# Kernel tuning notes

Measured on AMD Instinct MI355X. Metric: run time of the kernel, lower is better.

The kernel has to match this reference:

```python
import jax, jax.numpy as jnp
import numpy as np

N_NODES = 100000
N_EDGES = 3200000
N_GRAPHS = 128


def setup_inputs() -> dict:
    key = jax.random.key(0)
    ks = jax.random.split(key, 16)
    x = jax.random.normal(ks[0], (N_NODES, 47), dtype=jnp.float32)
    edge_index = jax.random.randint(ks[1], (2, N_EDGES), 0, N_NODES, dtype=jnp.int32)
    batch = jnp.sort(jax.random.randint(ks[2], (N_NODES,), 0, N_GRAPHS, dtype=jnp.int32))

    def w(k, shape):
        fan_in = shape[0]
        return jax.random.normal(k, shape, dtype=jnp.float32) * (1.0 / np.sqrt(fan_in))

    return {
        "x": x, "edge_index": edge_index, "batch": batch,
        "W1": w(ks[3], (47, 64)), "b1": jnp.zeros((64,), jnp.float32),
        "W2": w(ks[4], (64, 32)), "b2": jnp.zeros((32,), jnp.float32),
        "A1": w(ks[5], (32, 32)), "c1": jnp.zeros((32,), jnp.float32),
        "A2": w(ks[6], (32, 16)), "c2": jnp.zeros((16,), jnp.float32),
        "A3": w(ks[7], (16, 8)),  "c3": jnp.zeros((8,), jnp.float32),
        "A4": w(ks[8], (8, 1)),   "c4": jnp.zeros((1,), jnp.float32),
    }


def _gcn_conv(x, W, b, src, dst):
    # PyG GCNConv: h = XW, then D^-1/2 (A+I) D^-1/2 aggregation, then + bias.
    h = x @ W  # [N, out]
    ones = jnp.ones(dst.shape[0], dtype=h.dtype)
    deg = jax.ops.segment_sum(ones, dst, num_segments=N_NODES)  # incl. self loops
    dinv = jnp.where(deg > 0, jax.lax.rsqrt(deg), 0.0)
    norm = dinv[src] * dinv[dst]  # [E_total]
    msg = h[src] * norm[:, None]  # gather + normalize
    out = jax.ops.segment_sum(msg, dst, num_segments=N_NODES)  # scatter-add
    return out + b


def reference(x, edge_index, batch, W1, b1, W2, b2, A1, c1, A2, c2, A3, c3, A4, c4):
    loops = jnp.arange(N_NODES, dtype=edge_index.dtype)
    src = jnp.concatenate([edge_index[0], loops])
    dst = jnp.concatenate([edge_index[1], loops])
    h = jax.nn.relu(_gcn_conv(x, W1, b1, src, dst))
    h = jax.nn.relu(_gcn_conv(h, W2, b2, src, dst))
    # dropout is identity in eval mode
    g = jax.ops.segment_sum(h, batch, num_segments=N_GRAPHS)  # global_add_pool [G,32]
    g = jax.nn.relu(g @ A1 + c1)
    g = jax.nn.relu(g @ A2 + c2)
    g = jax.nn.relu(g @ A3 + c3)
    return g @ A4 + c4  # [G, 1]
```

## Files before the change

### kernel.cpp

```cpp
#include <hip/hip_runtime.h>

#define N_NODES 100000
#define N_EDGES 3200000
#define N_GRAPHS 128

#define RSHIFT 8
#define NPR 256
#define R_RANGES ((N_NODES + NPR - 1) / NPR)
#define CAP 9472
#define C_CHUNKS 512
#define EPC (N_EDGES / C_CHUNKS)
#define SRC_BITS 17

#define XPB 64
#define AXW 48

__device__ inline unsigned short f2bf(float f) {
    unsigned u = __float_as_uint(f);
    unsigned r = u + 0x7FFFu + ((u >> 16) & 1u);
    return (unsigned short)(r >> 16);
}
__device__ inline float bflo(unsigned u) { return __uint_as_float(u << 16); }
__device__ inline float bfhi(unsigned u) { return __uint_as_float(u & 0xFFFF0000u); }


__global__ __launch_bounds__(256) void padcvt_kernel(const float* __restrict__ x,
                                                     unsigned short* __restrict__ xpb,
                                                     int* __restrict__ range_next) {
    if (blockIdx.x < 2) {
        int i = blockIdx.x * 256 + threadIdx.x;
        if (i < R_RANGES) range_next[i] = i * CAP;
    }
    int idx = blockIdx.x * 256 + threadIdx.x;
    if (idx >= N_NODES * XPB) return;
    int n = idx >> 6;
    int c = idx & 63;
    float v = (c < 47) ? x[n * 47 + c] : 0.f;
    xpb[idx] = f2bf(v);
}


__global__ __launch_bounds__(256) void partition_kernel(const int* __restrict__ src,
                                                        const int* __restrict__ dst,
                                                        int* __restrict__ range_next,
                                                        int* __restrict__ bucket) {
    __shared__ int sorted[EPC];
    __shared__ unsigned short rid[EPC];
    __shared__ int cntL[R_RANGES];
    __shared__ int lstart[R_RANGES];
    __shared__ int baseL[R_RANGES];
    __shared__ int scanbuf[256];
    const int t = threadIdx.x, b = blockIdx.x;
    const int e0 = b * EPC;
    for (int i = t; i < R_RANGES; i += 256) cntL[i] = 0;
    __syncthreads();
    for (int i = t; i < EPC; i += 256) atomicAdd(&cntL[dst[e0 + i] >> RSHIFT], 1);
    __syncthreads();
    int i0 = 2 * t, i1 = 2 * t + 1;
    int v0 = (i0 < R_RANGES) ? cntL[i0] : 0;
    int v1 = (i1 < R_RANGES) ? cntL[i1] : 0;
    int s = v0 + v1;
    scanbuf[t] = s;
    __syncthreads();
    for (int d = 1; d < 256; d <<= 1) {
        int tv = (t >= d) ? scanbuf[t - d] : 0;
        __syncthreads();
        scanbuf[t] += tv;
        __syncthreads();
    }
    int ex = scanbuf[t] - s;
    if (i0 < R_RANGES) {
        lstart[i0] = ex;
        baseL[i0] = (v0 > 0) ? atomicAdd(&range_next[i0], v0) : 0;
        cntL[i0] = 0;
    }
    if (i1 < R_RANGES) {
        lstart[i1] = ex + v0;
        baseL[i1] = (v1 > 0) ? atomicAdd(&range_next[i1], v1) : 0;
        cntL[i1] = 0;
    }
    __syncthreads();
    for (int i = t; i < EPC; i += 256) {
        int d = dst[e0 + i];
        int sv = src[e0 + i];
        int r = d >> RSHIFT;
        int q = lstart[r] + atomicAdd(&cntL[r], 1);
        sorted[q] = ((d & (NPR - 1)) << SRC_BITS) | sv;
        rid[q] = (unsigned short)r;
    }
    __syncthreads();
    for (int i = t; i < EPC; i += 256) {
        int r = rid[i];
        bucket[baseL[r] + (i - lstart[r])] = sorted[i];
    }
}


__global__ __launch_bounds__(256) void build_kernel(const int* __restrict__ bucket,
                                                    const int* __restrict__ range_next,
                                                    int* __restrict__ row_ptr,
                                                    int* __restrict__ row_cnt,
                                                    float* __restrict__ dinv,
                                                    int* __restrict__ csr_src) {
    __shared__ int sE[CAP];
    __shared__ int degs[NPR];
    __shared__ int part[256];
    const int t = threadIdx.x, r = blockIdx.x;
    const int base_node = r * NPR;
    const int seg0 = r * CAP;
    int m = range_next[r] - seg0;
    if (m > CAP) m = CAP;
    for (int i = t; i < m; i += 256) sE[i] = bucket[seg0 + i];
    degs[t] = 0;
    __syncthreads();
    for (int i = t; i < m; i += 256) atomicAdd(&degs[sE[i] >> SRC_BITS], 1);
    __syncthreads();
    int d = degs[t];
    part[t] = d;
    __syncthreads();
    for (int dd = 1; dd < 256; dd <<= 1) {
        int tv = (t >= dd) ? part[t - dd] : 0;
        __syncthreads();
        part[t] += tv;
        __syncthreads();
    }
    int ex = part[t] - d;
    int node = base_node + t;
    if (node < N_NODES) {
        row_ptr[node] = seg0 + ex;
        row_cnt[node] = d;
        dinv[node] = rsqrtf((float)(d + 1));
    }
    degs[t] = ex;
    __syncthreads();
    for (int i = t; i < m; i += 256) {
        int p = sE[i];
        int pos = atomicAdd(&degs[p >> SRC_BITS], 1);
        csr_src[seg0 + pos] = p & ((1 << SRC_BITS) - 1);
    }
}


__global__ __launch_bounds__(256) void wprep_kernel(const int* __restrict__ csr_src,
                                                    const int* __restrict__ range_next,
                                                    const float* __restrict__ dinv,
                                                    float* __restrict__ csr_w) {
    const int t = threadIdx.x, r = blockIdx.x;
    const int seg0 = r * CAP;
    int m = range_next[r] - seg0;
    if (m > CAP) m = CAP;
    for (int i = t; i < m; i += 256) {
        csr_w[seg0 + i] = dinv[csr_src[seg0 + i]];
    }
}


__global__ __launch_bounds__(256) void aggX_kernel(const unsigned short* __restrict__ xpb,
                                                   const float* __restrict__ dinv,
                                                   const int* __restrict__ row_ptr,
                                                   const int* __restrict__ row_cnt,
                                                   const int* __restrict__ csr_src,
                                                   const float* __restrict__ csr_w,
                                                   unsigned short* __restrict__ aggxb) {
    const int tid = threadIdx.x;
    const int n = blockIdx.x * 4 + (tid >> 6);
    if (n >= N_NODES) return;
    const int l = tid & 63;
    const int eo = l >> 3;
    const int cg = l & 7;
    const float dn = dinv[n];

    float acc[8] = {0.f, 0.f, 0.f, 0.f, 0.f, 0.f, 0.f, 0.f};
    if (eo == 0) {
        uint4 q = *(const uint4*)(xpb + (size_t)n * XPB + cg * 8);
        float w = dn * dn;
        acc[0] = bflo(q.x) * w; acc[1] = bfhi(q.x) * w;
        acc[2] = bflo(q.y) * w; acc[3] = bfhi(q.y) * w;
        acc[4] = bflo(q.z) * w; acc[5] = bfhi(q.z) * w;
        acc[6] = bflo(q.w) * w; acc[7] = bfhi(q.w) * w;
    }
    const int st = row_ptr[n];
    const int cnt = row_cnt[n];
    int k = eo;
    for (; k + 8 < cnt; k += 16) {
        int s0 = csr_src[st + k];
        int s1 = csr_src[st + k + 8];
        float w0 = csr_w[st + k] * dn;
        float w1 = csr_w[st + k + 8] * dn;
        uint4 q0 = *(const uint4*)(xpb + (size_t)s0 * XPB + cg * 8);
        uint4 q1 = *(const uint4*)(xpb + (size_t)s1 * XPB + cg * 8);
        acc[0] = fmaf(bflo(q0.x), w0, acc[0]); acc[1] = fmaf(bfhi(q0.x), w0, acc[1]);
        acc[2] = fmaf(bflo(q0.y), w0, acc[2]); acc[3] = fmaf(bfhi(q0.y), w0, acc[3]);
        acc[4] = fmaf(bflo(q0.z), w0, acc[4]); acc[5] = fmaf(bfhi(q0.z), w0, acc[5]);
        acc[6] = fmaf(bflo(q0.w), w0, acc[6]); acc[7] = fmaf(bfhi(q0.w), w0, acc[7]);
        acc[0] = fmaf(bflo(q1.x), w1, acc[0]); acc[1] = fmaf(bfhi(q1.x), w1, acc[1]);
        acc[2] = fmaf(bflo(q1.y), w1, acc[2]); acc[3] = fmaf(bfhi(q1.y), w1, acc[3]);
        acc[4] = fmaf(bflo(q1.z), w1, acc[4]); acc[5] = fmaf(bfhi(q1.z), w1, acc[5]);
        acc[6] = fmaf(bflo(q1.w), w1, acc[6]); acc[7] = fmaf(bfhi(q1.w), w1, acc[7]);
    }
    if (k < cnt) {
        int s0 = csr_src[st + k];
        float w0 = csr_w[st + k] * dn;
        uint4 q0 = *(const uint4*)(xpb + (size_t)s0 * XPB + cg * 8);
        acc[0] = fmaf(bflo(q0.x), w0, acc[0]); acc[1] = fmaf(bfhi(q0.x), w0, acc[1]);
        acc[2] = fmaf(bflo(q0.y), w0, acc[2]); acc[3] = fmaf(bfhi(q0.y), w0, acc[3]);
        acc[4] = fmaf(bflo(q0.z), w0, acc[4]); acc[5] = fmaf(bfhi(q0.z), w0, acc[5]);
        acc[6] = fmaf(bflo(q0.w), w0, acc[6]); acc[7] = fmaf(bfhi(q0.w), w0, acc[7]);
    }
#pragma unroll
    for (int off = 8; off <= 32; off <<= 1) {
#pragma unroll
        for (int j = 0; j < 8; ++j) acc[j] += __shfl_xor(acc[j], off);
    }
    if (eo == 0 && cg < 6) {
        uint4 o;
        o.x = ((unsigned)f2bf(acc[1]) << 16) | f2bf(acc[0]);
        o.y = ((unsigned)f2bf(acc[3]) << 16) | f2bf(acc[2]);
        o.z = ((unsigned)f2bf(acc[5]) << 16) | f2bf(acc[4]);
        o.w = ((unsigned)f2bf(acc[7]) << 16) | f2bf(acc[6]);
        *(uint4*)(aggxb + (size_t)n * AXW + cg * 8) = o;
    }
}


#define FGW1 52
#define FGW2 68

__global__ __launch_bounds__(256) void fusedgemm_kernel(const unsigned short* __restrict__ aggxb,
                                                        const float* __restrict__ W1,
                                                        const float* __restrict__ b1,
                                                        const float* __restrict__ W2,
                                                        unsigned short* __restrict__ zb) {
    __shared__ float W1t[64 * FGW1];
    __shared__ float W2t[32 * FGW2];
    __shared__ float b1s[64];
    __shared__ float rows[4][4][48];
    __shared__ float ts[4][4][64];
    const int t = threadIdx.x;
    for (int i = t; i < 48 * 64; i += 256) { int k = i >> 6, c = i & 63; W1t[c * FGW1 + k] = W1[i]; }
    for (int i = t; i < 64 * 32; i += 256) { int k = i >> 5, c = i & 31; W2t[c * FGW2 + k] = W2[i]; }
    if (t < 64) b1s[t] = b1[t];
    __syncthreads();

    const int w = t >> 6, l = t & 63;
    const int nb0 = blockIdx.x * 64 + w * 16;
    const float* wc1 = &W1t[l * FGW1];
    const int nn = l >> 5, c2 = l & 31;
    const float* wc2 = &W2t[c2 * FGW2];

    for (int p = 0; p < 4; ++p) {
        const int n0 = nb0 + p * 4;
        if (n0 >= N_NODES) break;
        if (l < 48) {
#pragma unroll
            for (int j = 0; j < 4; ++j)
                rows[w][j][l] = bflo(aggxb[(size_t)(n0 + j) * AXW + l]);
        }
        {
            float h0 = b1s[l], h1 = h0, h2 = h0, h3 = h0;
#pragma unroll
            for (int k4 = 0; k4 < 48; k4 += 4) {
                float4 wv = *(const float4*)(wc1 + k4);
                float4 r0 = *(const float4*)&rows[w][0][k4];
                float4 r1 = *(const float4*)&rows[w][1][k4];
                float4 r2 = *(const float4*)&rows[w][2][k4];
                float4 r3 = *(const float4*)&rows[w][3][k4];
                h0 = fmaf(r0.x, wv.x, h0); h0 = fmaf(r0.y, wv.y, h0); h0 = fmaf(r0.z, wv.z, h0); h0 = fmaf(r0.w, wv.w, h0);
                h1 = fmaf(r1.x, wv.x, h1); h1 = fmaf(r1.y, wv.y, h1); h1 = fmaf(r1.z, wv.z, h1); h1 = fmaf(r1.w, wv.w, h1);
                h2 = fmaf(r2.x, wv.x, h2); h2 = fmaf(r2.y, wv.y, h2); h2 = fmaf(r2.z, wv.z, h2); h2 = fmaf(r2.w, wv.w, h2);
                h3 = fmaf(r3.x, wv.x, h3); h3 = fmaf(r3.y, wv.y, h3); h3 = fmaf(r3.z, wv.z, h3); h3 = fmaf(r3.w, wv.w, h3);
            }
            ts[w][0][l] = fmaxf(h0, 0.f);
            ts[w][1][l] = fmaxf(h1, 0.f);
            ts[w][2][l] = fmaxf(h2, 0.f);
            ts[w][3][l] = fmaxf(h3, 0.f);
        }
#pragma unroll
        for (int sp = 0; sp < 2; ++sp) {
            const float* tv = ts[w][sp * 2 + nn];
            float z = 0.f;
#pragma unroll
            for (int k4 = 0; k4 < 64; k4 += 4) {
                float4 a = *(const float4*)(tv + k4);
                float4 wv = *(const float4*)(wc2 + k4);
                z = fmaf(a.x, wv.x, z); z = fmaf(a.y, wv.y, z); z = fmaf(a.z, wv.z, z); z = fmaf(a.w, wv.w, z);
            }
            zb[(size_t)(n0 + sp * 2 + nn) * 32 + c2] = f2bf(z);
        }
    }
}


__global__ __launch_bounds__(256) void aggregate32_kernel(const unsigned short* __restrict__ zb,
                                                          const float* __restrict__ dinv,
                                                          const int* __restrict__ row_ptr,
                                                          const int* __restrict__ row_cnt,
                                                          const int* __restrict__ csr_src,
                                                          const float* __restrict__ csr_w,
                                                          const float* __restrict__ bias,
                                                          float* __restrict__ out) {
    const int tid = threadIdx.x;
    const int n = blockIdx.x * 4 + (tid >> 6);
    if (n >= N_NODES) return;
    const int l = tid & 63;
    const int eo = l >> 2;
    const int cg = l & 3;
    const float dn = dinv[n];

    float acc[8] = {0.f, 0.f, 0.f, 0.f, 0.f, 0.f, 0.f, 0.f};
    if (eo == 0) {
        uint4 q = *(const uint4*)(zb + (size_t)n * 32 + cg * 8);
        float w = dn * dn;
        acc[0] = bflo(q.x) * w; acc[1] = bfhi(q.x) * w;
        acc[2] = bflo(q.y) * w; acc[3] = bfhi(q.y) * w;
        acc[4] = bflo(q.z) * w; acc[5] = bfhi(q.z) * w;
        acc[6] = bflo(q.w) * w; acc[7] = bfhi(q.w) * w;
    }
    const int st = row_ptr[n];
    const int cnt = row_cnt[n];
    int k = eo;
    for (; k + 16 < cnt; k += 32) {
        int s0 = csr_src[st + k];
        int s1 = csr_src[st + k + 16];
        float w0 = csr_w[st + k] * dn;
        float w1 = csr_w[st + k + 16] * dn;
        uint4 q0 = *(const uint4*)(zb + (size_t)s0 * 32 + cg * 8);
        uint4 q1 = *(const uint4*)(zb + (size_t)s1 * 32 + cg * 8);
        acc[0] = fmaf(bflo(q0.x), w0, acc[0]); acc[1] = fmaf(bfhi(q0.x), w0, acc[1]);
        acc[2] = fmaf(bflo(q0.y), w0, acc[2]); acc[3] = fmaf(bfhi(q0.y), w0, acc[3]);
        acc[4] = fmaf(bflo(q0.z), w0, acc[4]); acc[5] = fmaf(bfhi(q0.z), w0, acc[5]);
        acc[6] = fmaf(bflo(q0.w), w0, acc[6]); acc[7] = fmaf(bfhi(q0.w), w0, acc[7]);
        acc[0] = fmaf(bflo(q1.x), w1, acc[0]); acc[1] = fmaf(bfhi(q1.x), w1, acc[1]);
        acc[2] = fmaf(bflo(q1.y), w1, acc[2]); acc[3] = fmaf(bfhi(q1.y), w1, acc[3]);
        acc[4] = fmaf(bflo(q1.z), w1, acc[4]); acc[5] = fmaf(bfhi(q1.z), w1, acc[5]);
        acc[6] = fmaf(bflo(q1.w), w1, acc[6]); acc[7] = fmaf(bfhi(q1.w), w1, acc[7]);
    }
    if (k < cnt) {
        int s0 = csr_src[st + k];
        float w0 = csr_w[st + k] * dn;
        uint4 q0 = *(const uint4*)(zb + (size_t)s0 * 32 + cg * 8);
        acc[0] = fmaf(bflo(q0.x), w0, acc[0]); acc[1] = fmaf(bfhi(q0.x), w0, acc[1]);
        acc[2] = fmaf(bflo(q0.y), w0, acc[2]); acc[3] = fmaf(bfhi(q0.y), w0, acc[3]);
        acc[4] = fmaf(bflo(q0.z), w0, acc[4]); acc[5] = fmaf(bfhi(q0.z), w0, acc[5]);
        acc[6] = fmaf(bflo(q0.w), w0, acc[6]); acc[7] = fmaf(bfhi(q0.w), w0, acc[7]);
    }
#pragma unroll
    for (int off = 4; off <= 32; off <<= 1) {
#pragma unroll
        for (int j = 0; j < 8; ++j) acc[j] += __shfl_xor(acc[j], off);
    }
    if (eo == 0) {
        const float* bp = bias + cg * 8;
        float4 a, b;
        a.x = fmaxf(acc[0] + bp[0], 0.f);
        a.y = fmaxf(acc[1] + bp[1], 0.f);
        a.z = fmaxf(acc[2] + bp[2], 0.f);
        a.w = fmaxf(acc[3] + bp[3], 0.f);
        b.x = fmaxf(acc[4] + bp[4], 0.f);
        b.y = fmaxf(acc[5] + bp[5], 0.f);
        b.z = fmaxf(acc[6] + bp[6], 0.f);
        b.w = fmaxf(acc[7] + bp[7], 0.f);
        *(float4*)(out + (size_t)n * 32 + cg * 8) = a;
        *(float4*)(out + (size_t)n * 32 + cg * 8 + 4) = b;
    }
}


#define POOL_NPB 256

__global__ __launch_bounds__(256) void pool_kernel(const int* __restrict__ batch,
                                                   const float* __restrict__ h,
                                                   float* __restrict__ g) {
    const int t = threadIdx.x;
    const int c = t & 31;
    const int r = t >> 5;
    int i0 = blockIdx.x * POOL_NPB;
    int i1 = i0 + POOL_NPB;
    if (i1 > N_NODES) i1 = N_NODES;
    int cur_g = -1;
    float acc = 0.f;
    for (int i = i0 + r; i < i1; i += 8) {
        int gi = batch[i];
        float v = h[(size_t)i * 32 + c];
        if (gi != cur_g) {
            if (cur_g >= 0) atomicAdd(&g[cur_g * 32 + c], acc);
            acc = 0.f;
            cur_g = gi;
        }
        acc += v;
    }
    if (cur_g >= 0) atomicAdd(&g[cur_g * 32 + c], acc);
}


__global__ __launch_bounds__(128) void mlp_kernel(const float* __restrict__ g,
                                                  const float* __restrict__ A1, const float* __restrict__ c1,
                                                  const float* __restrict__ A2, const float* __restrict__ c2,
                                                  const float* __restrict__ A3, const float* __restrict__ c3,
                                                  const float* __restrict__ A4, const float* __restrict__ c4,
                                                  float* __restrict__ out) {
    int t = threadIdx.x;
    float v[32];
#pragma unroll
    for (int k = 0; k < 32; ++k) v[k] = g[t * 32 + k];
    float u[32];
#pragma unroll
    for (int c = 0; c < 32; ++c) {
        float s = c1[c];
#pragma unroll
        for (int k = 0; k < 32; ++k) s = fmaf(v[k], A1[k * 32 + c], s);
        u[c] = fmaxf(s, 0.f);
    }
    float w[16];
#pragma unroll
    for (int c = 0; c < 16; ++c) {
        float s = c2[c];
#pragma unroll
        for (int k = 0; k < 32; ++k) s = fmaf(u[k], A2[k * 16 + c], s);
        w[c] = fmaxf(s, 0.f);
    }
    float z[8];
#pragma unroll
    for (int c = 0; c < 8; ++c) {
        float s = c3[c];
#pragma unroll
        for (int k = 0; k < 16; ++k) s = fmaf(w[k], A3[k * 8 + c], s);
        z[c] = fmaxf(s, 0.f);
    }
    float s = c4[0];
#pragma unroll
    for (int k = 0; k < 8; ++k) s = fmaf(z[k], A4[k], s);
    out[t] = s;
}


extern "C" void kernel_launch(void* const* d_in, const int* in_sizes, int n_in,
                              void* d_out, int out_size, void* d_ws, size_t ws_size,
                              hipStream_t stream) {
    const float* x    = (const float*)d_in[0];
    const int*   ei   = (const int*)d_in[1];
    const int*   srcE = ei;
    const int*   dstE = ei + N_EDGES;
    const int*   batch = (const int*)d_in[2];
    const float* W1 = (const float*)d_in[3];  const float* b1 = (const float*)d_in[4];
    const float* W2 = (const float*)d_in[5];  const float* b2 = (const float*)d_in[6];
    const float* A1 = (const float*)d_in[7];  const float* c1 = (const float*)d_in[8];
    const float* A2 = (const float*)d_in[9];  const float* c2 = (const float*)d_in[10];
    const float* A3 = (const float*)d_in[11]; const float* c3 = (const float*)d_in[12];
    const float* A4 = (const float*)d_in[13]; const float* c4 = (const float*)d_in[14];
    float* out = (float*)d_out;

    char* ws = (char*)d_ws;
    size_t off_b = 0;
    auto take = [&](size_t bytes) -> char* {
        char* p = ws + off_b;
        off_b = (off_b + bytes + 255) & ~(size_t)255;
        return p;
    };
    int*            row_ptr    = (int*)take((size_t)N_NODES * 4);
    int*            row_cnt    = (int*)take((size_t)N_NODES * 4);
    float*          dinv       = (float*)take((size_t)N_NODES * 4);
    int*            range_next = (int*)take((size_t)R_RANGES * 4);
    int*            csr_src    = (int*)take((size_t)R_RANGES * CAP * 4);
    float*          csr_w      = (float*)take((size_t)R_RANGES * CAP * 4);
    char*           bz_raw     = take((size_t)R_RANGES * CAP * 4);
    int*            bucket     = (int*)bz_raw;
    unsigned short* zb         = (unsigned short*)bz_raw;
    unsigned short* xpb        = (unsigned short*)take((size_t)N_NODES * XPB * 2);
    char*           aa_raw     = take((size_t)N_NODES * 32 * 4);
    unsigned short* aggxb      = (unsigned short*)aa_raw;
    float*          agg        = (float*)aa_raw;
    float*          g          = (float*)take((size_t)N_GRAPHS * 32 * 4);
    (void)ws_size; (void)in_sizes; (void)n_in; (void)out_size;

    padcvt_kernel<<<(N_NODES * XPB + 255) / 256, 256, 0, stream>>>(x, xpb, range_next);

    partition_kernel<<<C_CHUNKS, 256, 0, stream>>>(srcE, dstE, range_next, bucket);
    build_kernel<<<R_RANGES, 256, 0, stream>>>(bucket, range_next, row_ptr, row_cnt, dinv, csr_src);
    wprep_kernel<<<R_RANGES, 256, 0, stream>>>(csr_src, range_next, dinv, csr_w);

    aggX_kernel<<<(N_NODES + 3) / 4, 256, 0, stream>>>(xpb, dinv, row_ptr, row_cnt, csr_src, csr_w, aggxb);
    fusedgemm_kernel<<<(N_NODES + 63) / 64, 256, 0, stream>>>(aggxb, W1, b1, W2, zb);
    aggregate32_kernel<<<(N_NODES + 3) / 4, 256, 0, stream>>>(zb, dinv, row_ptr, row_cnt, csr_src, csr_w, b2, agg);

    hipMemsetAsync(g, 0, (size_t)N_GRAPHS * 32 * 4, stream);
    pool_kernel<<<(N_NODES + POOL_NPB - 1) / POOL_NPB, 256, 0, stream>>>(batch, agg, g);
    mlp_kernel<<<1, 128, 0, stream>>>(g, A1, c1, A2, c2, A3, c3, A4, c4, out);
}
```

Measured before the change: 385.2 us.

## Compute fused two-layer GEMM with one node per thread in registers

Result: slower. 400.1 us (+3.9%).

```diff
diff --git a/kernel.cpp b/kernel.cpp
--- a/kernel.cpp
+++ b/kernel.cpp
@@ -223,70 +223,38 @@
 }
 
 
-#define FGW1 52
-#define FGW2 68
-
-__global__ __launch_bounds__(256) void fusedgemm_kernel(const unsigned short* __restrict__ aggxb,
+__global__ __launch_bounds__(128) void fusedgemm_kernel(const unsigned short* __restrict__ aggxb,
                                                         const float* __restrict__ W1,
                                                         const float* __restrict__ b1,
                                                         const float* __restrict__ W2,
                                                         unsigned short* __restrict__ zb) {
-    __shared__ float W1t[64 * FGW1];
-    __shared__ float W2t[32 * FGW2];
-    __shared__ float b1s[64];
-    __shared__ float rows[4][4][48];
-    __shared__ float ts[4][4][64];
-    const int t = threadIdx.x;
-    for (int i = t; i < 48 * 64; i += 256) { int k = i >> 6, c = i & 63; W1t[c * FGW1 + k] = W1[i]; }
-    for (int i = t; i < 64 * 32; i += 256) { int k = i >> 5, c = i & 31; W2t[c * FGW2 + k] = W2[i]; }
-    if (t < 64) b1s[t] = b1[t];
-    __syncthreads();
-
-    const int w = t >> 6, l = t & 63;
-    const int nb0 = blockIdx.x * 64 + w * 16;
-    const float* wc1 = &W1t[l * FGW1];
-    const int nn = l >> 5, c2 = l & 31;
-    const float* wc2 = &W2t[c2 * FGW2];
-
-    for (int p = 0; p < 4; ++p) {
-        const int n0 = nb0 + p * 4;
-        if (n0 >= N_NODES) break;
-        if (l < 48) {
-#pragma unroll
-            for (int j = 0; j < 4; ++j)
-                rows[w][j][l] = bflo(aggxb[(size_t)(n0 + j) * AXW + l]);
+    const int n = blockIdx.x * 128 + threadIdx.x;
+    if (n >= N_NODES) return;
+    unsigned qa[24];
+    const unsigned* rp = (const unsigned*)(aggxb + (size_t)n * AXW);
+#pragma unroll
+    for (int i = 0; i < 24; ++i) qa[i] = rp[i];
+    float row[48];
+#pragma unroll
+    for (int i = 0; i < 24; ++i) { row[2 * i] = bflo(qa[i]); row[2 * i + 1] = bfhi(qa[i]); }
+    float h[64];
+#pragma unroll
+    for (int c = 0; c < 64; ++c) {
+        float s = b1[c];
+#pragma unroll
+        for (int k = 0; k < 48; ++k) s = fmaf(row[k], W1[k * 64 + c], s);
+        h[c] = fmaxf(s, 0.f);
+    }
+    unsigned* op = (unsigned*)(zb + (size_t)n * 32);
+#pragma unroll
+    for (int cp = 0; cp < 16; ++cp) {
+        float s0 = 0.f, s1 = 0.f;
+#pragma unroll
+        for (int k = 0; k < 64; ++k) {
+            s0 = fmaf(h[k], W2[k * 32 + 2 * cp], s0);
+            s1 = fmaf(h[k], W2[k * 32 + 2 * cp + 1], s1);
         }
-        {
-            float h0 = b1s[l], h1 = h0, h2 = h0, h3 = h0;
-#pragma unroll
-            for (int k4 = 0; k4 < 48; k4 += 4) {
-                float4 wv = *(const float4*)(wc1 + k4);
-                float4 r0 = *(const float4*)&rows[w][0][k4];
-                float4 r1 = *(const float4*)&rows[w][1][k4];
-                float4 r2 = *(const float4*)&rows[w][2][k4];
-                float4 r3 = *(const float4*)&rows[w][3][k4];
-                h0 = fmaf(r0.x, wv.x, h0); h0 = fmaf(r0.y, wv.y, h0); h0 = fmaf(r0.z, wv.z, h0); h0 = fmaf(r0.w, wv.w, h0);
-                h1 = fmaf(r1.x, wv.x, h1); h1 = fmaf(r1.y, wv.y, h1); h1 = fmaf(r1.z, wv.z, h1); h1 = fmaf(r1.w, wv.w, h1);
-                h2 = fmaf(r2.x, wv.x, h2); h2 = fmaf(r2.y, wv.y, h2); h2 = fmaf(r2.z, wv.z, h2); h2 = fmaf(r2.w, wv.w, h2);
-                h3 = fmaf(r3.x, wv.x, h3); h3 = fmaf(r3.y, wv.y, h3); h3 = fmaf(r3.z, wv.z, h3); h3 = fmaf(r3.w, wv.w, h3);
-            }
-            ts[w][0][l] = fmaxf(h0, 0.f);
-            ts[w][1][l] = fmaxf(h1, 0.f);
-            ts[w][2][l] = fmaxf(h2, 0.f);
-            ts[w][3][l] = fmaxf(h3, 0.f);
-        }
-#pragma unroll
-        for (int sp = 0; sp < 2; ++sp) {
-            const float* tv = ts[w][sp * 2 + nn];
-            float z = 0.f;
-#pragma unroll
-            for (int k4 = 0; k4 < 64; k4 += 4) {
-                float4 a = *(const float4*)(tv + k4);
-                float4 wv = *(const float4*)(wc2 + k4);
-                z = fmaf(a.x, wv.x, z); z = fmaf(a.y, wv.y, z); z = fmaf(a.z, wv.z, z); z = fmaf(a.w, wv.w, z);
-            }
-            zb[(size_t)(n0 + sp * 2 + nn) * 32 + c2] = f2bf(z);
-        }
+        op[cp] = ((unsigned)f2bf(s1) << 16) | f2bf(s0);
     }
 }
 
@@ -480,7 +448,7 @@
     wprep_kernel<<<R_RANGES, 256, 0, stream>>>(csr_src, range_next, dinv, csr_w);
 
     aggX_kernel<<<(N_NODES + 3) / 4, 256, 0, stream>>>(xpb, dinv, row_ptr, row_cnt, csr_src, csr_w, aggxb);
-    fusedgemm_kernel<<<(N_NODES + 63) / 64, 256, 0, stream>>>(aggxb, W1, b1, W2, zb);
+    fusedgemm_kernel<<<(N_NODES + 127) / 128, 128, 0, stream>>>(aggxb, W1, b1, W2, zb);
     aggregate32_kernel<<<(N_NODES + 3) / 4, 256, 0, stream>>>(zb, dinv, row_ptr, row_cnt, csr_src, csr_w, b2, agg);
 
     hipMemsetAsync(g, 0, (size_t)N_GRAPHS * 32 * 4, stream);
```
